# Performance work log

Hardware: AMD Instinct MI355X
Metric: run time of the kernel (lower is better)

The kernel has to match this reference:

```python
import jax, jax.numpy as jnp
import numpy as np

BS, S, D, H = 2, 2048, 1024, 16
DH = D // H  # 64


def setup_inputs() -> dict:
    key = jax.random.key(0)
    k1, k2, k3 = jax.random.split(key, 3)
    x = jax.random.normal(k1, (BS, S, D), dtype=jnp.float32)
    w_qkv = jax.random.normal(k2, (D, H, 3 * DH), dtype=jnp.float32) * (D ** -0.5)
    b_qkv = jnp.zeros((H, 3 * DH), dtype=jnp.float32)
    w_out = jax.random.normal(k3, (H, DH, D), dtype=jnp.float32) * (D ** -0.5)
    b_out = jnp.zeros((D,), dtype=jnp.float32)
    return {"x": x, "w_qkv": w_qkv, "b_qkv": b_qkv, "w_out": w_out, "b_out": b_out}


def reference(x, w_qkv, b_qkv, w_out, b_out):
    dtype = x.dtype
    # QKV projection: DenseGeneral(features=(H, 3*DH)) -> [B, S, H, 3*DH]
    qkv = jnp.einsum("bsd,dhf->bshf", x, w_qkv) + b_qkv
    q, k, v = jnp.split(qkv, 3, axis=-1)  # each [B, S, H, DH]

    scale = DH ** -0.5
    q = (q * scale).astype(jnp.float32)
    k = k.astype(jnp.float32)
    # Full causal attention with fp32 scores (as in original)
    weights = jnp.einsum("bqhd,bkhd->bhqk", q, k)  # [B, H, S, S]
    causal = jnp.tril(jnp.ones((S, S), dtype=bool))[None, None, :, :]
    weights = jnp.where(causal, weights, jnp.finfo(jnp.float32).min)
    weights = jax.nn.softmax(weights, axis=-1).astype(dtype)
    attn = jnp.einsum("bhqk,bkhd->bqhd", weights, v).astype(dtype)

    # Output projection: DenseGeneral(D, axis=(-2, -1))
    out = jnp.einsum("bqhd,hdo->bqo", attn, w_out) + b_out
    return out
```

## Files before the change

kernel.cpp:

```cpp
#include <hip/hip_runtime.h>
#include <hip/hip_bf16.h>
#include <stdint.h>

#define NBS 2
#define SEQ 2048
#define DMODEL 1024
#define NH 16
#define DHEAD 64
#define MROWS (NBS*SEQ)
#define NQKV (NH*3*DHEAD)

typedef __bf16 bf16;
typedef __bf16 bf16x8 __attribute__((ext_vector_type(8)));
typedef float f32x4 __attribute__((ext_vector_type(4)));
typedef float f32x16 __attribute__((ext_vector_type(16)));
typedef unsigned int u32x2 __attribute__((ext_vector_type(2)));

#define LOG2E 1.44269504088896f
#define QSCALE (0.125f * LOG2E)

static __device__ __forceinline__ void gload_lds16(const bf16* g, bf16* l) {
    __builtin_amdgcn_global_load_lds(
        (const __attribute__((address_space(1))) uint32_t*)g,
        (__attribute__((address_space(3))) uint32_t*)l, 16, 0, 0);
}

static __device__ __forceinline__ bf16x8 ld_b8(const bf16* p) {
    return __builtin_bit_cast(bf16x8, *(const uint4*)p);
}

static __device__ __forceinline__ uint32_t pk_bf16(float lo, float hi) {
    unsigned short l = __builtin_bit_cast(unsigned short, (bf16)lo);
    unsigned short h = __builtin_bit_cast(unsigned short, (bf16)hi);
    return ((uint32_t)h << 16) | (uint32_t)l;
}

static __device__ __forceinline__ u32x2 lane_swap32(uint32_t a, uint32_t b, int lane) {
#if __has_builtin(__builtin_amdgcn_permlane32_swap)
    return __builtin_amdgcn_permlane32_swap(a, b, false, false);
#else
    uint32_t sa = __shfl_xor(a, 32), sb = __shfl_xor(b, 32);
    u32x2 r;
    r.x = (lane >= 32) ? sb : a;
    r.y = (lane >= 32) ? b : sa;
    return r;
#endif
}


__global__ void k_cvt(const float* __restrict__ in, bf16* __restrict__ out, int n4) {
    int i = blockIdx.x * blockDim.x + threadIdx.x;
    if (i < n4) {
        float4 v = ((const float4*)in)[i];
        ushort4 o;
        o.x = __builtin_bit_cast(unsigned short, (bf16)v.x);
        o.y = __builtin_bit_cast(unsigned short, (bf16)v.y);
        o.z = __builtin_bit_cast(unsigned short, (bf16)v.z);
        o.w = __builtin_bit_cast(unsigned short, (bf16)v.w);
        ((ushort4*)out)[i] = o;
    }
}

__global__ void k_tcvt(const float* __restrict__ in, bf16* __restrict__ out, int R, int C) {
    __shared__ float t[32][33];
    int tx = threadIdx.x, ty = threadIdx.y;
    int r0 = blockIdx.y * 32, c0 = blockIdx.x * 32;
#pragma unroll
    for (int i = 0; i < 4; i++)
        t[ty + i*8][tx] = in[(size_t)(r0 + ty + i*8) * C + (c0 + tx)];
    __syncthreads();
#pragma unroll
    for (int i = 0; i < 4; i++)
        out[(size_t)(c0 + ty + i*8) * R + (r0 + tx)] = (bf16)t[tx][ty + i*8];
}

__global__ void k_tcvt_qkv(const float* __restrict__ in, bf16* __restrict__ out) {
    __shared__ float t[32][33];
    int tx = threadIdx.x, ty = threadIdx.y;
    int r0 = blockIdx.y * 32, c0 = blockIdx.x * 32;
#pragma unroll
    for (int i = 0; i < 4; i++)
        t[ty + i*8][tx] = in[(size_t)(r0 + ty + i*8) * NQKV + (c0 + tx)];
    __syncthreads();
#pragma unroll
    for (int i = 0; i < 4; i++) {
        int c = c0 + ty + i*8;
        int h = c / 192, f = c % 192;
        int cperm = ((f >> 6) << 10) + (h << 6) + (f & 63);
        out[(size_t)cperm * DMODEL + (r0 + tx)] = (bf16)t[tx][ty + i*8];
    }
}

#define G1_NT 16

__global__ __launch_bounds__(512, 2) void k_gemm_qkv(
        const bf16* __restrict__ A, const bf16* __restrict__ Bt,
        const float* __restrict__ bias,
        bf16* __restrict__ Q, bf16* __restrict__ Kp, bf16* __restrict__ Vt) {
    __shared__ __align__(16) bf16 As[2][256*64];
    __shared__ __align__(16) bf16 Bs[2][256*64];
    int tid = threadIdx.x;
    int wid = tid >> 6, lane = tid & 63;
    int wr = wid >> 2, wc = wid & 3;
    int g = lane >> 4, r = lane & 15;

    int lid = blockIdx.y * 12 + blockIdx.x;
    int swz = (lid & 7) * 24 + (lid >> 3);
    int tile_n = (swz % 12) * 256, tile_m = (swz / 12) * 256;

    f32x4 acc[8][4];
#pragma unroll
    for (int m = 0; m < 8; m++)
#pragma unroll
        for (int n = 0; n < 4; n++)
            acc[m][n] = (f32x4){0.f, 0.f, 0.f, 0.f};

    int srow[4], schk[4];
#pragma unroll
    for (int j2 = 0; j2 < 4; j2++) {
        int idx = tid + j2 * 512;
        srow[j2] = idx >> 3;
        schk[j2] = ((idx & 7) ^ (srow[j2] & 7)) * 8;
    }

#define G1_STAGE(buf, k0)                                                        \
    {                                                                            \
        _Pragma("unroll")                                                        \
        for (int j2 = 0; j2 < 4; j2++) {                                         \
            gload_lds16(A  + (size_t)(tile_m + srow[j2]) * DMODEL + (k0) + schk[j2], \
                        As[buf] + (tid + j2*512) * 8);                           \
            gload_lds16(Bt + (size_t)(tile_n + srow[j2]) * DMODEL + (k0) + schk[j2], \
                        Bs[buf] + (tid + j2*512) * 8);                           \
        }                                                                        \
    }

    G1_STAGE(0, 0);

    int r7 = r & 7;
    for (int t = 0; t < G1_NT; t++) {
        int cur = t & 1;
        if (t + 1 < G1_NT) {
            G1_STAGE(cur ^ 1, (t + 1) * 64);
            asm volatile("s_waitcnt vmcnt(8)" ::: "memory");
        } else {
            asm volatile("s_waitcnt vmcnt(0)" ::: "memory");
        }
        __builtin_amdgcn_s_barrier();
        __builtin_amdgcn_sched_barrier(0);

        const bf16* pa = As[cur];
        const bf16* pb = Bs[cur];
#pragma unroll
        for (int kk = 0; kk < 2; kk++) {
            int rchk = ((kk*4 + g) ^ r7) * 8;
            bf16x8 bfr[4];
#pragma unroll
            for (int n = 0; n < 4; n++)
                bfr[n] = ld_b8(pb + (wc*64 + n*16 + r) * 64 + rchk);
#pragma unroll
            for (int m = 0; m < 8; m++) {
                bf16x8 af = ld_b8(pa + (wr*128 + m*16 + r) * 64 + rchk);
#pragma unroll
                for (int n = 0; n < 4; n++)
                    acc[m][n] = __builtin_amdgcn_mfma_f32_16x16x32_bf16(af, bfr[n], acc[m][n], 0, 0, 0);
            }
        }
        asm volatile("s_waitcnt lgkmcnt(0)" ::: "memory");
        __builtin_amdgcn_s_barrier();
    }

#pragma unroll
    for (int m = 0; m < 8; m++) {
#pragma unroll
        for (int n = 0; n < 4; n++) {
            int col = tile_n + wc*64 + n*16 + r;
            int kind = col >> 10;
            int h = (col >> 6) & 15;
            int d = col & 63;
            float bv = bias[h*192 + (kind << 6) + d];
            if (kind == 2) {
                int row0 = tile_m + wr*128 + m*16 + g*4;
                int b = row0 >> 11, s0 = row0 & 2047;
                ushort4 vv;
                vv.x = __builtin_bit_cast(unsigned short, (bf16)(acc[m][n][0] + bv));
                vv.y = __builtin_bit_cast(unsigned short, (bf16)(acc[m][n][1] + bv));
                vv.z = __builtin_bit_cast(unsigned short, (bf16)(acc[m][n][2] + bv));
                vv.w = __builtin_bit_cast(unsigned short, (bf16)(acc[m][n][3] + bv));
                *(ushort4*)&Vt[(((size_t)(b*NH + h)) * DHEAD + d) * SEQ + s0] = vv;
            } else {
#pragma unroll
                for (int j = 0; j < 4; j++) {
                    int row = tile_m + wr*128 + m*16 + g*4 + j;
                    int b = row >> 11, s = row & 2047;
                    float v = acc[m][n][j] + bv;
                    size_t addr = (((size_t)(b*NH + h)) * SEQ + s) * DHEAD + d;
                    if (kind == 0) Q[addr]  = (bf16)(v * QSCALE);
                    else           Kp[addr] = (bf16)v;
                }
            }
        }
    }
#undef G1_STAGE
}

__global__ __launch_bounds__(256) void k_gemm_out(
        const bf16* __restrict__ A, const bf16* __restrict__ Bt,
        const float* __restrict__ bias, float* __restrict__ out) {
    __shared__ __align__(16) bf16 As[64*32];
    __shared__ __align__(16) bf16 Bs[128*32];
    int tid = threadIdx.x;
    int wave = tid >> 6, lane = tid & 63;
    int g = lane >> 4, r = lane & 15;
    int srow = lane >> 2, schunk = (lane & 3) * 8;
    int tile_m = blockIdx.y * 64, tile_n = blockIdx.x * 128;

    f32x4 acc[4][2];
#pragma unroll
    for (int m = 0; m < 4; m++)
#pragma unroll
        for (int n = 0; n < 2; n++)
            acc[m][n] = (f32x4){0.f, 0.f, 0.f, 0.f};

    for (int k0 = 0; k0 < DMODEL; k0 += 32) {
        gload_lds16(A  + (size_t)(tile_m + wave*16 + srow) * DMODEL + k0 + schunk, As + wave*512);
        gload_lds16(Bt + (size_t)(tile_n + wave*16 + srow) * DMODEL + k0 + schunk, Bs + wave*512);
        gload_lds16(Bt + (size_t)(tile_n + 64 + wave*16 + srow) * DMODEL + k0 + schunk, Bs + 2048 + wave*512);
        __syncthreads();
        bf16x8 af[4], bfr[2];
#pragma unroll
        for (int m = 0; m < 4; m++) af[m]  = *(const bf16x8*)(As + (m*16 + r)*32 + g*8);
#pragma unroll
        for (int n = 0; n < 2; n++) bfr[n] = *(const bf16x8*)(Bs + (wave*32 + n*16 + r)*32 + g*8);
#pragma unroll
        for (int m = 0; m < 4; m++)
#pragma unroll
            for (int n = 0; n < 2; n++)
                acc[m][n] = __builtin_amdgcn_mfma_f32_16x16x32_bf16(af[m], bfr[n], acc[m][n], 0, 0, 0);
        __syncthreads();
    }

#pragma unroll
    for (int m = 0; m < 4; m++) {
#pragma unroll
        for (int n = 0; n < 2; n++) {
            int col = tile_n + wave*32 + n*16 + r;
            float bv = bias[col];
#pragma unroll
            for (int j = 0; j < 4; j++) {
                int row = tile_m + m*16 + g*4 + j;
                out[(size_t)row * DMODEL + col] = acc[m][n][j] + bv;
            }
        }
    }
}

#define QBLK 128
#define KVB 64

static __device__ __forceinline__ void attn_tile_body(
        const bf16* Ks, const bf16* VsT,
        const bf16x8 qa2[4], const bf16x8& ones,
        f32x16 o32[2], f32x16& acc_l,
        int kv0, int qb, int qrow, int l31, int hi, int lane) {
    const f32x16 z16 = {0,0,0,0,0,0,0,0,0,0,0,0,0,0,0,0};
    int sw = (l31 & 7) << 3;
    f32x16 st[2];
    st[0] = z16; st[1] = z16;
    __builtin_amdgcn_s_setprio(1);
#pragma unroll
    for (int rb = 0; rb < 2; rb++) {
#pragma unroll
        for (int c = 0; c < 4; c++) {
            bf16x8 kf = ld_b8(Ks + ((((rb*32 + l31)*64) + c*16 + hi*8) ^ sw));
            st[rb] = __builtin_amdgcn_mfma_f32_32x32x16_bf16(kf, qa2[c], st[rb], 0, 0, 0);
        }
    }
    __builtin_amdgcn_s_setprio(0);

    bf16x8 vf[2][4];
#pragma unroll
    for (int dblk = 0; dblk < 2; dblk++)
#pragma unroll
        for (int c = 0; c < 4; c++)
            vf[dblk][c] = ld_b8(VsT + ((((dblk*32 + l31)*64) + c*16 + hi*8) ^ sw));

    bool needm = (kv0 + KVB - 1) > qb;
#pragma unroll
    for (int rb = 0; rb < 2; rb++) {
#pragma unroll
        for (int reg = 0; reg < 16; reg++) {
            float e = __builtin_amdgcn_exp2f(st[rb][reg]);
            if (needm) {
                int kv = kv0 + rb*32 + (reg & 3) + 8*(reg >> 2) + 4*hi;
                if (kv > qrow) e = 0.f;
            }
            st[rb][reg] = e;
        }
    }

    bf16x8 pa[4];
#pragma unroll
    for (int c = 0; c < 4; c++) {
        const f32x16& pp = st[c >> 1];
        const int base = (c & 1) * 8;
        uint32_t a0 = pk_bf16(pp[base+0], pp[base+1]);
        uint32_t a1 = pk_bf16(pp[base+2], pp[base+3]);
        uint32_t b0 = pk_bf16(pp[base+4], pp[base+5]);
        uint32_t b1 = pk_bf16(pp[base+6], pp[base+7]);
        u32x2 s0 = lane_swap32(a0, b0, lane);
        u32x2 s1 = lane_swap32(a1, b1, lane);
        uint4 fr = {s0.x, s1.x, s0.y, s1.y};
        pa[c] = __builtin_bit_cast(bf16x8, fr);
    }

    __builtin_amdgcn_s_setprio(1);
#pragma unroll
    for (int dblk = 0; dblk < 2; dblk++)
#pragma unroll
        for (int c = 0; c < 4; c++)
            o32[dblk] = __builtin_amdgcn_mfma_f32_32x32x16_bf16(pa[c], vf[dblk][c], o32[dblk], 0, 0, 0);
#pragma unroll
    for (int c = 0; c < 4; c++)
        acc_l = __builtin_amdgcn_mfma_f32_32x32x16_bf16(pa[c], ones, acc_l, 0, 0, 0);
    __builtin_amdgcn_s_setprio(0);
}

__device__ const int8_t JQC[32]  = {10,10, 4, 0, 15,15, 3, 1,  9, 9, 7, 2, 13,14, 7, 5,
                                    14,14,11, 5, 15, 8,11, 6,  8,12,12, 6, 13,13,11,12};
__device__ const int8_t JT0[32]  = { 0,11, 0, 0,  0,11, 0, 0,  0,10, 0, 0,  0, 0, 8, 0,
                                    10,20, 0, 6, 22, 0, 8, 0,  9, 0, 9, 7, 10,19,16,18};
__device__ const int8_t JT1[32]  = {11,22,10, 2, 11,22, 8, 4, 10,20, 8, 6, 10,10,16, 6,
                                    20,30, 8,12, 32, 9,16, 7, 18, 9,18,14, 19,28,24,26};
__device__ const int8_t JSEG[32] = { 0, 1, 0, 0,  0, 1, 0, 0,  0, 1, 0, 0,  0, 0, 1, 0,
                                     1, 2, 0, 1,  2, 0, 1, 0,  1, 0, 1, 1,  1, 2, 2, 2};

__global__ __launch_bounds__(256) void k_attn_split(
        const bf16* __restrict__ Q, const bf16* __restrict__ K,
        const bf16* __restrict__ Vt,
        bf16* __restrict__ Op0, bf16* __restrict__ Op1, bf16* __restrict__ Op2,
        float* __restrict__ Lp0, float* __restrict__ Lp1, float* __restrict__ Lp2) {
    int scu = blockIdx.x;
    int bh = scu >> 3, slot = scu & 7;
    int j = slot * 4 + blockIdx.y;
    int qc  = JQC[j];
    int t0  = JT0[j];
    int t1  = JT1[j];
    int seg = JSEG[j];
    int q0 = qc * QBLK;
    int tid = threadIdx.x, wave = tid >> 6, lane = tid & 63;
    int l31 = lane & 31, hi = lane >> 5;

    __shared__ __align__(16) bf16 Ks[2][KVB*64];
    __shared__ __align__(16) bf16 VsT[2][KVB*64];

    const bf16* Kg = K  + (size_t)bh * SEQ * DHEAD;
    const bf16* Vg = Vt + (size_t)bh * DHEAD * SEQ;

    int qb = q0 + wave * 32;
    int qrow = qb + l31;

    const bf16* qrow_p = Q + ((size_t)bh * SEQ + qrow) * DHEAD;
    bf16x8 qa2[4];
#pragma unroll
    for (int c = 0; c < 4; c++) qa2[c] = ld_b8(qrow_p + c*16 + hi*8);

    bf16x8 ones;
#pragma unroll
    for (int c = 0; c < 8; c++) ones[c] = (bf16)1.0f;

    const f32x16 z16 = {0,0,0,0,0,0,0,0,0,0,0,0,0,0,0,0};
    f32x16 o32[2], acc_l;
    o32[0] = z16; o32[1] = z16; acc_l = z16;

    int qmax_wave = qb + 31;

    int srow = tid >> 3, sc8 = tid & 7;
    int sw_st = (srow & 7) << 3;
    int wK0 = ((srow*64)      + sc8*8) ^ sw_st;
    int wK1 = (((srow+32)*64) + sc8*8) ^ sw_st;

    bf16x8 kreg[2], vreg[2];
    {
        int kvs = t0 * KVB;
        kreg[0] = ld_b8(Kg + (size_t)(kvs + srow)      * DHEAD + sc8*8);
        kreg[1] = ld_b8(Kg + (size_t)(kvs + srow + 32) * DHEAD + sc8*8);
        vreg[0] = ld_b8(Vg + (size_t)srow      * SEQ + kvs + sc8*8);
        vreg[1] = ld_b8(Vg + (size_t)(srow+32) * SEQ + kvs + sc8*8);
    }

    int cur = 0;
    for (int t = t0; t < t1; t++) {
        int kv0 = t * KVB;
        *(uint4*)&Ks[cur][wK0]  = __builtin_bit_cast(uint4, kreg[0]);
        *(uint4*)&Ks[cur][wK1]  = __builtin_bit_cast(uint4, kreg[1]);
        *(uint4*)&VsT[cur][wK0] = __builtin_bit_cast(uint4, vreg[0]);
        *(uint4*)&VsT[cur][wK1] = __builtin_bit_cast(uint4, vreg[1]);
        __syncthreads();

        if (t + 1 < t1) {
            int kv1 = kv0 + KVB;
            kreg[0] = ld_b8(Kg + (size_t)(kv1 + srow)      * DHEAD + sc8*8);
            kreg[1] = ld_b8(Kg + (size_t)(kv1 + srow + 32) * DHEAD + sc8*8);
            vreg[0] = ld_b8(Vg + (size_t)srow      * SEQ + kv1 + sc8*8);
            vreg[1] = ld_b8(Vg + (size_t)(srow+32) * SEQ + kv1 + sc8*8);
        }

        if (kv0 <= qmax_wave)
            attn_tile_body(Ks[cur], VsT[cur], qa2, ones, o32, acc_l,
                           kv0, qb, qrow, l31, hi, lane);
        cur ^= 1;
    }

    bf16* Op; float* Lp; size_t obase; int lbase;
    if (seg == 0)      { Op = Op0; Lp = Lp0; obase = ((size_t)bh*2048 + q0) * 64;          lbase = bh*2048 + q0; }
    else if (seg == 1) { Op = Op1; Lp = Lp1; obase = ((size_t)bh*1408 + (qc-5)*128) * 64;  lbase = bh*1408 + (qc-5)*128; }
    else               { Op = Op2; Lp = Lp2; obase = ((size_t)bh*640  + (qc-11)*128) * 64; lbase = bh*640  + (qc-11)*128; }

    if (l31 == 0) {
#pragma unroll
        for (int reg = 0; reg < 16; reg++) {
            int qr = (reg & 3) + 8*(reg >> 2) + 4*hi;
            Lp[lbase + wave*32 + qr] = acc_l[reg];
        }
    }

#pragma unroll
    for (int reg = 0; reg < 16; reg++) {
        int qr = (reg & 3) + 8*(reg >> 2) + 4*hi;
        size_t base = obase + (size_t)(wave*32 + qr) * 64 + l31;
        Op[base]      = (bf16)o32[0][reg];
        Op[base + 32] = (bf16)o32[1][reg];
    }
}

__global__ __launch_bounds__(256) void k_merge(
        const bf16* __restrict__ Op0, const bf16* __restrict__ Op1,
        const bf16* __restrict__ Op2,
        const float* __restrict__ Lp0, const float* __restrict__ Lp1,
        const float* __restrict__ Lp2,
        bf16* __restrict__ Oa) {
    int g = blockIdx.x * 256 + threadIdx.x;
    int dseg = g & 7;
    int s = (g >> 3) & 2047;
    int bh = g >> 14;
    int qc = s >> 7;
    int sl = s & 127;

    size_t r0 = ((size_t)bh * 2048 + s) * 64 + dseg*8;
    bf16x8 p0 = ld_b8(Op0 + r0);
    float l = Lp0[bh*2048 + s];
    float acc[8];
#pragma unroll
    for (int i = 0; i < 8; i++) acc[i] = (float)p0[i];

    if (qc >= 5) {
        size_t r1 = ((size_t)bh * 1408 + (qc-5)*128 + sl) * 64 + dseg*8;
        bf16x8 p1 = ld_b8(Op1 + r1);
        l += Lp1[bh*1408 + (qc-5)*128 + sl];
#pragma unroll
        for (int i = 0; i < 8; i++) acc[i] += (float)p1[i];
        if (qc >= 11) {
            size_t r2 = ((size_t)bh * 640 + (qc-11)*128 + sl) * 64 + dseg*8;
            bf16x8 p2 = ld_b8(Op2 + r2);
            l += Lp2[bh*640 + (qc-11)*128 + sl];
#pragma unroll
            for (int i = 0; i < 8; i++) acc[i] += (float)p2[i];
        }
    }

    float inv = 1.0f / l;
    bf16x8 r;
#pragma unroll
    for (int i = 0; i < 8; i++) r[i] = (bf16)(acc[i] * inv);
    int b = bh >> 4, h = bh & 15;
    *(uint4*)&Oa[(((size_t)b * SEQ + s) * NH + h) * DHEAD + dseg*8] =
        __builtin_bit_cast(uint4, r);
}

__global__ __launch_bounds__(256) void k_attn(
        const bf16* __restrict__ Q, const bf16* __restrict__ K,
        const bf16* __restrict__ Vt, bf16* __restrict__ O) {
    int bh = blockIdx.y;
    int qc = (bh >= 16) ? (15 - (int)blockIdx.x) : (int)blockIdx.x;
    int q0 = qc * QBLK;
    int tid = threadIdx.x, wave = tid >> 6, lane = tid & 63;
    int l31 = lane & 31, hi = lane >> 5;

    __shared__ __align__(16) bf16 Ks[2][KVB*64];
    __shared__ __align__(16) bf16 VsT[2][KVB*64];

    const bf16* Kg = K  + (size_t)bh * SEQ * DHEAD;
    const bf16* Vg = Vt + (size_t)bh * DHEAD * SEQ;

    int qb = q0 + wave * 32;
    int qrow = qb + l31;

    const bf16* qrow_p = Q + ((size_t)bh * SEQ + qrow) * DHEAD;
    bf16x8 qa2[4];
#pragma unroll
    for (int c = 0; c < 4; c++) qa2[c] = ld_b8(qrow_p + c*16 + hi*8);

    bf16x8 ones;
#pragma unroll
    for (int c = 0; c < 8; c++) ones[c] = (bf16)1.0f;

    const f32x16 z16 = {0,0,0,0,0,0,0,0,0,0,0,0,0,0,0,0};
    f32x16 o32[2], acc_l;
    o32[0] = z16; o32[1] = z16; acc_l = z16;

    int nt = 2*qc + 2;
    int qmax_wave = qb + 31;

    int srow = tid >> 3, sc8 = tid & 7;
    int sw_st = (srow & 7) << 3;
    int wK0 = ((srow*64)      + sc8*8) ^ sw_st;
    int wK1 = (((srow+32)*64) + sc8*8) ^ sw_st;

    bf16x8 kreg[2], vreg[2];
    kreg[0] = ld_b8(Kg + (size_t)srow      * DHEAD + sc8*8);
    kreg[1] = ld_b8(Kg + (size_t)(srow+32) * DHEAD + sc8*8);
    vreg[0] = ld_b8(Vg + (size_t)srow      * SEQ + sc8*8);
    vreg[1] = ld_b8(Vg + (size_t)(srow+32) * SEQ + sc8*8);

    int cur = 0;
    for (int t = 0; t < nt; t++) {
        int kv0 = t * KVB;
        *(uint4*)&Ks[cur][wK0]  = __builtin_bit_cast(uint4, kreg[0]);
        *(uint4*)&Ks[cur][wK1]  = __builtin_bit_cast(uint4, kreg[1]);
        *(uint4*)&VsT[cur][wK0] = __builtin_bit_cast(uint4, vreg[0]);
        *(uint4*)&VsT[cur][wK1] = __builtin_bit_cast(uint4, vreg[1]);
        __syncthreads();

        if (t + 1 < nt) {
            int kv1 = kv0 + KVB;
            kreg[0] = ld_b8(Kg + (size_t)(kv1 + srow)      * DHEAD + sc8*8);
            kreg[1] = ld_b8(Kg + (size_t)(kv1 + srow + 32) * DHEAD + sc8*8);
            vreg[0] = ld_b8(Vg + (size_t)srow      * SEQ + kv1 + sc8*8);
            vreg[1] = ld_b8(Vg + (size_t)(srow+32) * SEQ + kv1 + sc8*8);
        }

        if (kv0 <= qmax_wave)
            attn_tile_body(Ks[cur], VsT[cur], qa2, ones, o32, acc_l,
                           kv0, qb, qrow, l31, hi, lane);
        cur ^= 1;
    }

    int b = bh >> 4, h = bh & 15;
#pragma unroll
    for (int reg = 0; reg < 16; reg++) {
        int qr = (reg & 3) + 8*(reg >> 2) + 4*hi;
        int srow2 = q0 + wave*32 + qr;
        float linv = 1.0f / acc_l[reg];
        size_t base = (((size_t)b * SEQ + srow2) * NH + h) * DHEAD + l31;
        O[base]      = (bf16)(o32[0][reg] * linv);
        O[base + 32] = (bf16)(o32[1][reg] * linv);
    }
}


extern "C" void kernel_launch(void* const* d_in, const int* in_sizes, int n_in,
                              void* d_out, int out_size, void* d_ws, size_t ws_size,
                              hipStream_t stream) {
    const float* x     = (const float*)d_in[0];
    const float* w_qkv = (const float*)d_in[1];
    const float* b_qkv = (const float*)d_in[2];
    const float* w_out = (const float*)d_in[3];
    const float* b_out = (const float*)d_in[4];
    float* out = (float*)d_out;

    char* ws = (char*)d_ws;
    bf16* xb   = (bf16*)(ws);
    bf16* wqkT = (bf16*)(ws + 8388608);
    bf16* woT  = (bf16*)(ws + 14680064);
    bf16* qb   = (bf16*)(ws + 16777216);
    bf16* kb   = (bf16*)(ws + 25165824);
    bf16* vb   = (bf16*)(ws + 33554432);
    bf16* Op0  = (bf16*)(ws + 41943040);
    bf16* Op1  = (bf16*)(ws + 50331648);
    bf16* Op2  = (bf16*)(ws + 56098816);
    float* Lp0 = (float*)(ws + 8388608);
    float* Lp1 = (float*)(ws + 8388608 + 262144);
    float* Lp2 = (float*)(ws + 8388608 + 524288);
    const size_t WS_NEED = 58720256;
    bf16* attn = xb;

    k_cvt<<<(MROWS*DMODEL/4 + 255)/256, 256, 0, stream>>>(x, xb, MROWS*DMODEL/4);
    dim3 tb(32, 8);
    k_tcvt_qkv<<<dim3(NQKV/32, DMODEL/32), tb, 0, stream>>>(w_qkv, wqkT);
    k_tcvt<<<dim3(DMODEL/32, DMODEL/32), tb, 0, stream>>>(w_out, woT, DMODEL, DMODEL);

    k_gemm_qkv<<<dim3(12, 16), 512, 0, stream>>>(xb, wqkT, b_qkv, qb, kb, vb);

    if (ws_size >= WS_NEED) {
        k_attn_split<<<dim3(256, 4), 256, 0, stream>>>(qb, kb, vb,
                                                       Op0, Op1, Op2, Lp0, Lp1, Lp2);
        k_merge<<<(NBS*NH*SEQ*DHEAD/8)/256, 256, 0, stream>>>(Op0, Op1, Op2,
                                                              Lp0, Lp1, Lp2, attn);
    } else {
        k_attn<<<dim3(SEQ/QBLK, NBS*NH), 256, 0, stream>>>(qb, kb, vb, attn);
    }

    k_gemm_out<<<dim3(DMODEL/128, MROWS/64), 256, 0, stream>>>(attn, woT, b_out, out);
}
```

Baseline: 120.9 us.

## Stage 128-key K/V tiles via direct global-to-LDS loads and batch two QK blocks

Both attention kernels drop the register-staged double buffer. They now load a 128-key K/V tile straight into LDS with global_load_lds, using an XOR swizzle. Each staged tile holds two 64-key sub-blocks, and both QK products are issued back to back before the softmax/PV steps to give more MFMA work per barrier. V fragments are read from LDS inside the PV loop, the masked and unmasked exp paths are split, and launch bounds request 3 blocks per CU. The trade-off is that global loads no longer overlap compute across iterations (load, sync, compute, sync), and register pressure may rise from keeping two score tiles live.

Result: slower. 132.9 us (+9.9%).

```diff
diff --git a/kernel.cpp b/kernel.cpp
--- a/kernel.cpp
+++ b/kernel.cpp
@@ -257,45 +257,41 @@
 #define QBLK 128
 #define KVB 64
 
-static __device__ __forceinline__ void attn_tile_body(
-        const bf16* Ks, const bf16* VsT,
-        const bf16x8 qa2[4], const bf16x8& ones,
+static __device__ __forceinline__ void a_qk(
+        const bf16* KsL, const bf16x8 qa2[4], f32x16 st[2], int s, int l31, int hi) {
+    int sw = (l31 & 7) << 3;
+    __builtin_amdgcn_s_setprio(1);
+#pragma unroll
+    for (int rb = 0; rb < 2; rb++)
+#pragma unroll
+        for (int c = 0; c < 4; c++) {
+            bf16x8 kf = ld_b8(KsL + (s*64 + rb*32 + l31)*64 + ((c*16 + hi*8) ^ sw));
+            st[rb] = __builtin_amdgcn_mfma_f32_32x32x16_bf16(kf, qa2[c], st[rb], 0, 0, 0);
+        }
+    __builtin_amdgcn_s_setprio(0);
+}
+
+static __device__ __forceinline__ void a_rest(
+        const bf16* VsL, f32x16 st[2], const bf16x8& ones,
         f32x16 o32[2], f32x16& acc_l,
-        int kv0, int qb, int qrow, int l31, int hi, int lane) {
-    const f32x16 z16 = {0,0,0,0,0,0,0,0,0,0,0,0,0,0,0,0};
-    int sw = (l31 & 7) << 3;
-    f32x16 st[2];
-    st[0] = z16; st[1] = z16;
-    __builtin_amdgcn_s_setprio(1);
-#pragma unroll
-    for (int rb = 0; rb < 2; rb++) {
-#pragma unroll
-        for (int c = 0; c < 4; c++) {
-            bf16x8 kf = ld_b8(Ks + ((((rb*32 + l31)*64) + c*16 + hi*8) ^ sw));
-            st[rb] = __builtin_amdgcn_mfma_f32_32x32x16_bf16(kf, qa2[c], st[rb], 0, 0, 0);
-        }
-    }
-    __builtin_amdgcn_s_setprio(0);
-
-    bf16x8 vf[2][4];
-#pragma unroll
-    for (int dblk = 0; dblk < 2; dblk++)
-#pragma unroll
-        for (int c = 0; c < 4; c++)
-            vf[dblk][c] = ld_b8(VsT + ((((dblk*32 + l31)*64) + c*16 + hi*8) ^ sw));
-
-    bool needm = (kv0 + KVB - 1) > qb;
-#pragma unroll
-    for (int rb = 0; rb < 2; rb++) {
-#pragma unroll
-        for (int reg = 0; reg < 16; reg++) {
-            float e = __builtin_amdgcn_exp2f(st[rb][reg]);
-            if (needm) {
-                int kv = kv0 + rb*32 + (reg & 3) + 8*(reg >> 2) + 4*hi;
+        int s, int kvb, int qb, int qrow, int l31, int hi, int lane) {
+    bool needm = (kvb + KVB - 1) > qb;
+    if (needm) {
+#pragma unroll
+        for (int rb = 0; rb < 2; rb++)
+#pragma unroll
+            for (int reg = 0; reg < 16; reg++) {
+                float e = __builtin_amdgcn_exp2f(st[rb][reg]);
+                int kv = kvb + rb*32 + (reg & 3) + 8*(reg >> 2) + 4*hi;
                 if (kv > qrow) e = 0.f;
+                st[rb][reg] = e;
             }
-            st[rb][reg] = e;
-        }
+    } else {
+#pragma unroll
+        for (int rb = 0; rb < 2; rb++)
+#pragma unroll
+            for (int reg = 0; reg < 16; reg++)
+                st[rb][reg] = __builtin_amdgcn_exp2f(st[rb][reg]);
     }
 
     bf16x8 pa[4];
@@ -313,12 +309,15 @@
         pa[c] = __builtin_bit_cast(bf16x8, fr);
     }
 
+    int sw = (l31 & 7) << 3;
     __builtin_amdgcn_s_setprio(1);
 #pragma unroll
     for (int dblk = 0; dblk < 2; dblk++)
 #pragma unroll
-        for (int c = 0; c < 4; c++)
-            o32[dblk] = __builtin_amdgcn_mfma_f32_32x32x16_bf16(pa[c], vf[dblk][c], o32[dblk], 0, 0, 0);
+        for (int c = 0; c < 4; c++) {
+            bf16x8 vf = ld_b8(VsL + (dblk*32 + l31)*128 + ((s*64 + c*16 + hi*8) ^ sw));
+            o32[dblk] = __builtin_amdgcn_mfma_f32_32x32x16_bf16(pa[c], vf, o32[dblk], 0, 0, 0);
+        }
 #pragma unroll
     for (int c = 0; c < 4; c++)
         acc_l = __builtin_amdgcn_mfma_f32_32x32x16_bf16(pa[c], ones, acc_l, 0, 0, 0);
@@ -334,7 +333,7 @@
 __device__ const int8_t JSEG[32] = { 0, 1, 0, 0,  0, 1, 0, 0,  0, 1, 0, 0,  0, 0, 1, 0,
                                      1, 2, 0, 1,  2, 0, 1, 0,  1, 0, 1, 1,  1, 2, 2, 2};
 
-__global__ __launch_bounds__(256) void k_attn_split(
+__global__ __launch_bounds__(256, 3) void k_attn_split(
         const bf16* __restrict__ Q, const bf16* __restrict__ K,
         const bf16* __restrict__ Vt,
         bf16* __restrict__ Op0, bf16* __restrict__ Op1, bf16* __restrict__ Op2,
@@ -350,8 +349,8 @@
     int tid = threadIdx.x, wave = tid >> 6, lane = tid & 63;
     int l31 = lane & 31, hi = lane >> 5;
 
-    __shared__ __align__(16) bf16 Ks[2][KVB*64];
-    __shared__ __align__(16) bf16 VsT[2][KVB*64];
+    __shared__ __align__(16) bf16 KsL[128*64];
+    __shared__ __align__(16) bf16 VsL[64*128];
 
     const bf16* Kg = K  + (size_t)bh * SEQ * DHEAD;
     const bf16* Vg = Vt + (size_t)bh * DHEAD * SEQ;
@@ -374,42 +373,45 @@
 
     int qmax_wave = qb + 31;
 
-    int srow = tid >> 3, sc8 = tid & 7;
-    int sw_st = (srow & 7) << 3;
-    int wK0 = ((srow*64)      + sc8*8) ^ sw_st;
-    int wK1 = (((srow+32)*64) + sc8*8) ^ sw_st;
-
-    bf16x8 kreg[2], vreg[2];
-    {
-        int kvs = t0 * KVB;
-        kreg[0] = ld_b8(Kg + (size_t)(kvs + srow)      * DHEAD + sc8*8);
-        kreg[1] = ld_b8(Kg + (size_t)(kvs + srow + 32) * DHEAD + sc8*8);
-        vreg[0] = ld_b8(Vg + (size_t)srow      * SEQ + kvs + sc8*8);
-        vreg[1] = ld_b8(Vg + (size_t)(srow+32) * SEQ + kvs + sc8*8);
-    }
-
-    int cur = 0;
-    for (int t = t0; t < t1; t++) {
-        int kv0 = t * KVB;
-        *(uint4*)&Ks[cur][wK0]  = __builtin_bit_cast(uint4, kreg[0]);
-        *(uint4*)&Ks[cur][wK1]  = __builtin_bit_cast(uint4, kreg[1]);
-        *(uint4*)&VsT[cur][wK0] = __builtin_bit_cast(uint4, vreg[0]);
-        *(uint4*)&VsT[cur][wK1] = __builtin_bit_cast(uint4, vreg[1]);
+#define A_STAGE(kv0s)                                                     \
+    {                                                                     \
+        _Pragma("unroll")                                                 \
+        for (int i = 0; i < 4; i++) {                                     \
+            int c2 = tid + i*256;                                         \
+            int krow = c2 >> 3;                                           \
+            int kch = ((c2 & 7) ^ (krow & 7)) * 8;                        \
+            int kgr = (kv0s) + krow; if (kgr > SEQ-1) kgr = SEQ-1;        \
+            gload_lds16(Kg + (size_t)kgr * DHEAD + kch, KsL + c2*8);      \
+            int vrow = c2 >> 4;                                           \
+            int vch = ((c2 & 15) ^ (vrow & 7)) * 8;                       \
+            int vgc = (kv0s) + vch; if (vgc > SEQ-8) vgc = SEQ-8;         \
+            gload_lds16(Vg + (size_t)vrow * SEQ + vgc, VsL + c2*8);       \
+        }                                                                 \
+    }
+
+    for (int t = t0; t < t1; t += 2) {
+        A_STAGE(t * KVB);
         __syncthreads();
-
-        if (t + 1 < t1) {
-            int kv1 = kv0 + KVB;
-            kreg[0] = ld_b8(Kg + (size_t)(kv1 + srow)      * DHEAD + sc8*8);
-            kreg[1] = ld_b8(Kg + (size_t)(kv1 + srow + 32) * DHEAD + sc8*8);
-            vreg[0] = ld_b8(Vg + (size_t)srow      * SEQ + kv1 + sc8*8);
-            vreg[1] = ld_b8(Vg + (size_t)(srow+32) * SEQ + kv1 + sc8*8);
-        }
-
-        if (kv0 <= qmax_wave)
-            attn_tile_body(Ks[cur], VsT[cur], qa2, ones, o32, acc_l,
-                           kv0, qb, qrow, l31, hi, lane);
-        cur ^= 1;
-    }
+        int kv00 = t * KVB;
+        bool a1 = (t + 1 < t1) && (kv00 + KVB <= qmax_wave);
+        if (kv00 <= qmax_wave) {
+            f32x16 sa[2];
+            sa[0] = z16; sa[1] = z16;
+            if (a1) {
+                f32x16 sb[2];
+                sb[0] = z16; sb[1] = z16;
+                a_qk(KsL, qa2, sa, 0, l31, hi);
+                a_qk(KsL, qa2, sb, 1, l31, hi);
+                a_rest(VsL, sa, ones, o32, acc_l, 0, kv00,     qb, qrow, l31, hi, lane);
+                a_rest(VsL, sb, ones, o32, acc_l, 1, kv00+KVB, qb, qrow, l31, hi, lane);
+            } else {
+                a_qk(KsL, qa2, sa, 0, l31, hi);
+                a_rest(VsL, sa, ones, o32, acc_l, 0, kv00, qb, qrow, l31, hi, lane);
+            }
+        }
+        __syncthreads();
+    }
+#undef A_STAGE
 
     bf16* Op; float* Lp; size_t obase; int lbase;
     if (seg == 0)      { Op = Op0; Lp = Lp0; obase = ((size_t)bh*2048 + q0) * 64;          lbase = bh*2048 + q0; }
@@ -477,7 +479,7 @@
         __builtin_bit_cast(uint4, r);
 }
 
-__global__ __launch_bounds__(256) void k_attn(
+__global__ __launch_bounds__(256, 3) void k_attn(
         const bf16* __restrict__ Q, const bf16* __restrict__ K,
         const bf16* __restrict__ Vt, bf16* __restrict__ O) {
     int bh = blockIdx.y;
@@ -486,8 +488,8 @@
     int tid = threadIdx.x, wave = tid >> 6, lane = tid & 63;
     int l31 = lane & 31, hi = lane >> 5;
 
-    __shared__ __align__(16) bf16 Ks[2][KVB*64];
-    __shared__ __align__(16) bf16 VsT[2][KVB*64];
+    __shared__ __align__(16) bf16 KsL[128*64];
+    __shared__ __align__(16) bf16 VsL[64*128];
 
     const bf16* Kg = K  + (size_t)bh * SEQ * DHEAD;
     const bf16* Vg = Vt + (size_t)bh * DHEAD * SEQ;
@@ -511,39 +513,45 @@
     int nt = 2*qc + 2;
     int qmax_wave = qb + 31;
 
-    int srow = tid >> 3, sc8 = tid & 7;
-    int sw_st = (srow & 7) << 3;
-    int wK0 = ((srow*64)      + sc8*8) ^ sw_st;
-    int wK1 = (((srow+32)*64) + sc8*8) ^ sw_st;
-
-    bf16x8 kreg[2], vreg[2];
-    kreg[0] = ld_b8(Kg + (size_t)srow      * DHEAD + sc8*8);
-    kreg[1] = ld_b8(Kg + (size_t)(srow+32) * DHEAD + sc8*8);
-    vreg[0] = ld_b8(Vg + (size_t)srow      * SEQ + sc8*8);
-    vreg[1] = ld_b8(Vg + (size_t)(srow+32) * SEQ + sc8*8);
-
-    int cur = 0;
-    for (int t = 0; t < nt; t++) {
-        int kv0 = t * KVB;
-        *(uint4*)&Ks[cur][wK0]  = __builtin_bit_cast(uint4, kreg[0]);
-        *(uint4*)&Ks[cur][wK1]  = __builtin_bit_cast(uint4, kreg[1]);
-        *(uint4*)&VsT[cur][wK0] = __builtin_bit_cast(uint4, vreg[0]);
-        *(uint4*)&VsT[cur][wK1] = __builtin_bit_cast(uint4, vreg[1]);
+#define A_STAGE(kv0s)                                                     \
+    {                                                                     \
+        _Pragma("unroll")                                                 \
+        for (int i = 0; i < 4; i++) {                                     \
+            int c2 = tid + i*256;                                         \
+            int krow = c2 >> 3;                                           \
+            int kch = ((c2 & 7) ^ (krow & 7)) * 8;                        \
+            int kgr = (kv0s) + krow; if (kgr > SEQ-1) kgr = SEQ-1;        \
+            gload_lds16(Kg + (size_t)kgr * DHEAD + kch, KsL + c2*8);      \
+            int vrow = c2 >> 4;                                           \
+            int vch = ((c2 & 15) ^ (vrow & 7)) * 8;                       \
+            int vgc = (kv0s) + vch; if (vgc > SEQ-8) vgc = SEQ-8;         \
+            gload_lds16(Vg + (size_t)vrow * SEQ + vgc, VsL + c2*8);       \
+        }                                                                 \
+    }
+
+    for (int t = 0; t < nt; t += 2) {
+        A_STAGE(t * KVB);
         __syncthreads();
-
-        if (t + 1 < nt) {
-            int kv1 = kv0 + KVB;
-            kreg[0] = ld_b8(Kg + (size_t)(kv1 + srow)      * DHEAD + sc8*8);
-            kreg[1] = ld_b8(Kg + (size_t)(kv1 + srow + 32) * DHEAD + sc8*8);
-            vreg[0] = ld_b8(Vg + (size_t)srow      * SEQ + kv1 + sc8*8);
-            vreg[1] = ld_b8(Vg + (size_t)(srow+32) * SEQ + kv1 + sc8*8);
-        }
-
-        if (kv0 <= qmax_wave)
-            attn_tile_body(Ks[cur], VsT[cur], qa2, ones, o32, acc_l,
-                           kv0, qb, qrow, l31, hi, lane);
-        cur ^= 1;
-    }
+        int kv00 = t * KVB;
+        bool a1 = (t + 1 < nt) && (kv00 + KVB <= qmax_wave);
+        if (kv00 <= qmax_wave) {
+            f32x16 sa[2];
+            sa[0] = z16; sa[1] = z16;
+            if (a1) {
+                f32x16 sb[2];
+                sb[0] = z16; sb[1] = z16;
+                a_qk(KsL, qa2, sa, 0, l31, hi);
+                a_qk(KsL, qa2, sb, 1, l31, hi);
+                a_rest(VsL, sa, ones, o32, acc_l, 0, kv00,     qb, qrow, l31, hi, lane);
+                a_rest(VsL, sb, ones, o32, acc_l, 1, kv00+KVB, qb, qrow, l31, hi, lane);
+            } else {
+                a_qk(KsL, qa2, sa, 0, l31, hi);
+                a_rest(VsL, sa, ones, o32, acc_l, 0, kv00, qb, qrow, l31, hi, lane);
+            }
+        }
+        __syncthreads();
+    }
+#undef A_STAGE
 
     int b = bh >> 4, h = bh & 15;
 #pragma unroll
```

## Stage attention K/V tiles via direct global-to-LDS async loads

Applied to the files above, without the earlier changes.

Replaces the register-staged K/V prefetch (global load into VGPRs, then an LDS store) in both attention kernels with global_load_lds DMA writes directly into the swizzled double-buffered LDS tiles. Synchronisation now uses explicit vmcnt waits plus raw barriers. The tile body is split into QK and softmax/PV parts, and V fragments are loaded from LDS just before each MFMA instead of up front. This frees VGPRs and removes the LDS store instructions, at the cost of an extra barrier per iteration and more delicate wait-count correctness.

Result: slower. 124.9 us (+3.3%).

```diff
diff --git a/kernel.cpp b/kernel.cpp
--- a/kernel.cpp
+++ b/kernel.cpp
@@ -257,46 +257,36 @@
 #define QBLK 128
 #define KVB 64
 
-static __device__ __forceinline__ void attn_tile_body(
-        const bf16* Ks, const bf16* VsT,
-        const bf16x8 qa2[4], const bf16x8& ones,
+static __device__ __forceinline__ void a_qk(
+        const bf16* Ks, const bf16x8 qa2[4], f32x16 st[2], int l31, int hi) {
+    int sw = (l31 & 7) << 3;
+    __builtin_amdgcn_s_setprio(1);
+#pragma unroll
+    for (int rb = 0; rb < 2; rb++)
+#pragma unroll
+        for (int c = 0; c < 4; c++) {
+            bf16x8 kf = ld_b8(Ks + (rb*32 + l31)*64 + ((c*16 + hi*8) ^ sw));
+            st[rb] = __builtin_amdgcn_mfma_f32_32x32x16_bf16(kf, qa2[c], st[rb], 0, 0, 0);
+        }
+    __builtin_amdgcn_s_setprio(0);
+}
+
+static __device__ __forceinline__ void a_rest(
+        const bf16* VsT, f32x16 st[2], const bf16x8& ones,
         f32x16 o32[2], f32x16& acc_l,
-        int kv0, int qb, int qrow, int l31, int hi, int lane) {
-    const f32x16 z16 = {0,0,0,0,0,0,0,0,0,0,0,0,0,0,0,0};
-    int sw = (l31 & 7) << 3;
-    f32x16 st[2];
-    st[0] = z16; st[1] = z16;
-    __builtin_amdgcn_s_setprio(1);
-#pragma unroll
-    for (int rb = 0; rb < 2; rb++) {
-#pragma unroll
-        for (int c = 0; c < 4; c++) {
-            bf16x8 kf = ld_b8(Ks + ((((rb*32 + l31)*64) + c*16 + hi*8) ^ sw));
-            st[rb] = __builtin_amdgcn_mfma_f32_32x32x16_bf16(kf, qa2[c], st[rb], 0, 0, 0);
-        }
-    }
-    __builtin_amdgcn_s_setprio(0);
-
-    bf16x8 vf[2][4];
-#pragma unroll
-    for (int dblk = 0; dblk < 2; dblk++)
-#pragma unroll
-        for (int c = 0; c < 4; c++)
-            vf[dblk][c] = ld_b8(VsT + ((((dblk*32 + l31)*64) + c*16 + hi*8) ^ sw));
-
-    bool needm = (kv0 + KVB - 1) > qb;
-#pragma unroll
-    for (int rb = 0; rb < 2; rb++) {
+        int kvb, int qb, int qrow, int l31, int hi, int lane) {
+    bool needm = (kvb + KVB - 1) > qb;
+#pragma unroll
+    for (int rb = 0; rb < 2; rb++)
 #pragma unroll
         for (int reg = 0; reg < 16; reg++) {
             float e = __builtin_amdgcn_exp2f(st[rb][reg]);
             if (needm) {
-                int kv = kv0 + rb*32 + (reg & 3) + 8*(reg >> 2) + 4*hi;
+                int kv = kvb + rb*32 + (reg & 3) + 8*(reg >> 2) + 4*hi;
                 if (kv > qrow) e = 0.f;
             }
             st[rb][reg] = e;
         }
-    }
 
     bf16x8 pa[4];
 #pragma unroll
@@ -313,12 +303,15 @@
         pa[c] = __builtin_bit_cast(bf16x8, fr);
     }
 
+    int sw = (l31 & 7) << 3;
     __builtin_amdgcn_s_setprio(1);
 #pragma unroll
     for (int dblk = 0; dblk < 2; dblk++)
 #pragma unroll
-        for (int c = 0; c < 4; c++)
-            o32[dblk] = __builtin_amdgcn_mfma_f32_32x32x16_bf16(pa[c], vf[dblk][c], o32[dblk], 0, 0, 0);
+        for (int c = 0; c < 4; c++) {
+            bf16x8 vf = ld_b8(VsT + (dblk*32 + l31)*64 + ((c*16 + hi*8) ^ sw));
+            o32[dblk] = __builtin_amdgcn_mfma_f32_32x32x16_bf16(pa[c], vf, o32[dblk], 0, 0, 0);
+        }
 #pragma unroll
     for (int c = 0; c < 4; c++)
         acc_l = __builtin_amdgcn_mfma_f32_32x32x16_bf16(pa[c], ones, acc_l, 0, 0, 0);
@@ -374,42 +367,42 @@
 
     int qmax_wave = qb + 31;
 
-    int srow = tid >> 3, sc8 = tid & 7;
-    int sw_st = (srow & 7) << 3;
-    int wK0 = ((srow*64)      + sc8*8) ^ sw_st;
-    int wK1 = (((srow+32)*64) + sc8*8) ^ sw_st;
-
-    bf16x8 kreg[2], vreg[2];
-    {
-        int kvs = t0 * KVB;
-        kreg[0] = ld_b8(Kg + (size_t)(kvs + srow)      * DHEAD + sc8*8);
-        kreg[1] = ld_b8(Kg + (size_t)(kvs + srow + 32) * DHEAD + sc8*8);
-        vreg[0] = ld_b8(Vg + (size_t)srow      * SEQ + kvs + sc8*8);
-        vreg[1] = ld_b8(Vg + (size_t)(srow+32) * SEQ + kvs + sc8*8);
-    }
-
-    int cur = 0;
+    int c2a = tid, c2b = tid + 256;
+    int rowA = c2a >> 3, chA = ((c2a & 7) ^ (rowA & 7)) * 8;
+    int rowB = c2b >> 3, chB = ((c2b & 7) ^ (rowB & 7)) * 8;
+
+#define A_STAGE(buf, kv0s)                                                    \
+    {                                                                         \
+        gload_lds16(Kg + (size_t)((kv0s) + rowA) * DHEAD + chA, Ks[buf] + c2a*8);  \
+        gload_lds16(Kg + (size_t)((kv0s) + rowB) * DHEAD + chB, Ks[buf] + c2b*8);  \
+        gload_lds16(Vg + (size_t)rowA * SEQ + (kv0s) + chA, VsT[buf] + c2a*8);     \
+        gload_lds16(Vg + (size_t)rowB * SEQ + (kv0s) + chB, VsT[buf] + c2b*8);     \
+    }
+
+    A_STAGE(0, t0 * KVB);
+
     for (int t = t0; t < t1; t++) {
+        int cur = (t - t0) & 1;
+        if (t + 1 < t1) {
+            A_STAGE(cur ^ 1, (t + 1) * KVB);
+            asm volatile("s_waitcnt vmcnt(4)" ::: "memory");
+        } else {
+            asm volatile("s_waitcnt vmcnt(0)" ::: "memory");
+        }
+        __builtin_amdgcn_s_barrier();
+        __builtin_amdgcn_sched_barrier(0);
+
         int kv0 = t * KVB;
-        *(uint4*)&Ks[cur][wK0]  = __builtin_bit_cast(uint4, kreg[0]);
-        *(uint4*)&Ks[cur][wK1]  = __builtin_bit_cast(uint4, kreg[1]);
-        *(uint4*)&VsT[cur][wK0] = __builtin_bit_cast(uint4, vreg[0]);
-        *(uint4*)&VsT[cur][wK1] = __builtin_bit_cast(uint4, vreg[1]);
-        __syncthreads();
-
-        if (t + 1 < t1) {
-            int kv1 = kv0 + KVB;
-            kreg[0] = ld_b8(Kg + (size_t)(kv1 + srow)      * DHEAD + sc8*8);
-            kreg[1] = ld_b8(Kg + (size_t)(kv1 + srow + 32) * DHEAD + sc8*8);
-            vreg[0] = ld_b8(Vg + (size_t)srow      * SEQ + kv1 + sc8*8);
-            vreg[1] = ld_b8(Vg + (size_t)(srow+32) * SEQ + kv1 + sc8*8);
-        }
-
-        if (kv0 <= qmax_wave)
-            attn_tile_body(Ks[cur], VsT[cur], qa2, ones, o32, acc_l,
-                           kv0, qb, qrow, l31, hi, lane);
-        cur ^= 1;
-    }
+        if (kv0 <= qmax_wave) {
+            f32x16 st[2];
+            st[0] = z16; st[1] = z16;
+            a_qk(Ks[cur], qa2, st, l31, hi);
+            a_rest(VsT[cur], st, ones, o32, acc_l, kv0, qb, qrow, l31, hi, lane);
+        }
+        asm volatile("s_waitcnt lgkmcnt(0)" ::: "memory");
+        __builtin_amdgcn_s_barrier();
+    }
+#undef A_STAGE
 
     bf16* Op; float* Lp; size_t obase; int lbase;
     if (seg == 0)      { Op = Op0; Lp = Lp0; obase = ((size_t)bh*2048 + q0) * 64;          lbase = bh*2048 + q0; }
@@ -511,39 +504,42 @@
     int nt = 2*qc + 2;
     int qmax_wave = qb + 31;
 
-    int srow = tid >> 3, sc8 = tid & 7;
-    int sw_st = (srow & 7) << 3;
-    int wK0 = ((srow*64)      + sc8*8) ^ sw_st;
-    int wK1 = (((srow+32)*64) + sc8*8) ^ sw_st;
-
-    bf16x8 kreg[2], vreg[2];
-    kreg[0] = ld_b8(Kg + (size_t)srow      * DHEAD + sc8*8);
-    kreg[1] = ld_b8(Kg + (size_t)(srow+32) * DHEAD + sc8*8);
-    vreg[0] = ld_b8(Vg + (size_t)srow      * SEQ + sc8*8);
-    vreg[1] = ld_b8(Vg + (size_t)(srow+32) * SEQ + sc8*8);
-
-    int cur = 0;
+    int c2a = tid, c2b = tid + 256;
+    int rowA = c2a >> 3, chA = ((c2a & 7) ^ (rowA & 7)) * 8;
+    int rowB = c2b >> 3, chB = ((c2b & 7) ^ (rowB & 7)) * 8;
+
+#define A_STAGE(buf, kv0s)                                                    \
+    {                                                                         \
+        gload_lds16(Kg + (size_t)((kv0s) + rowA) * DHEAD + chA, Ks[buf] + c2a*8);  \
+        gload_lds16(Kg + (size_t)((kv0s) + rowB) * DHEAD + chB, Ks[buf] + c2b*8);  \
+        gload_lds16(Vg + (size_t)rowA * SEQ + (kv0s) + chA, VsT[buf] + c2a*8);     \
+        gload_lds16(Vg + (size_t)rowB * SEQ + (kv0s) + chB, VsT[buf] + c2b*8);     \
+    }
+
+    A_STAGE(0, 0);
+
     for (int t = 0; t < nt; t++) {
+        int cur = t & 1;
+        if (t + 1 < nt) {
+            A_STAGE(cur ^ 1, (t + 1) * KVB);
+            asm volatile("s_waitcnt vmcnt(4)" ::: "memory");
+        } else {
+            asm volatile("s_waitcnt vmcnt(0)" ::: "memory");
+        }
+        __builtin_amdgcn_s_barrier();
+        __builtin_amdgcn_sched_barrier(0);
+
         int kv0 = t * KVB;
-        *(uint4*)&Ks[cur][wK0]  = __builtin_bit_cast(uint4, kreg[0]);
-        *(uint4*)&Ks[cur][wK1]  = __builtin_bit_cast(uint4, kreg[1]);
-        *(uint4*)&VsT[cur][wK0] = __builtin_bit_cast(uint4, vreg[0]);
-        *(uint4*)&VsT[cur][wK1] = __builtin_bit_cast(uint4, vreg[1]);
-        __syncthreads();
-
-        if (t + 1 < nt) {
-            int kv1 = kv0 + KVB;
-            kreg[0] = ld_b8(Kg + (size_t)(kv1 + srow)      * DHEAD + sc8*8);
-            kreg[1] = ld_b8(Kg + (size_t)(kv1 + srow + 32) * DHEAD + sc8*8);
-            vreg[0] = ld_b8(Vg + (size_t)srow      * SEQ + kv1 + sc8*8);
-            vreg[1] = ld_b8(Vg + (size_t)(srow+32) * SEQ + kv1 + sc8*8);
-        }
-
-        if (kv0 <= qmax_wave)
-            attn_tile_body(Ks[cur], VsT[cur], qa2, ones, o32, acc_l,
-                           kv0, qb, qrow, l31, hi, lane);
-        cur ^= 1;
-    }
+        if (kv0 <= qmax_wave) {
+            f32x16 st[2];
+            st[0] = z16; st[1] = z16;
+            a_qk(Ks[cur], qa2, st, l31, hi);
+            a_rest(VsT[cur], st, ones, o32, acc_l, kv0, qb, qrow, l31, hi, lane);
+        }
+        asm volatile("s_waitcnt lgkmcnt(0)" ::: "memory");
+        __builtin_amdgcn_s_barrier();
+    }
+#undef A_STAGE
 
     int b = bh >> 4, h = bh & 15;
 #pragma unroll
```
